# Optimization experiments

Measured on AMD Instinct MI355X. Metric: run time of the kernel, lower is better.

## Reference

```python
import math
import jax, jax.numpy as jnp
import numpy as np

L = 16
LOG2T = 19
T = 1 << LOG2T
FDIM = 2
N_MIN = 16
N_MAX = 512
N_PTS = 1 << 20
B_GROWTH = math.exp((math.log(N_MAX) - math.log(N_MIN)) / (L - 1))
RESOLUTIONS = [math.floor(N_MIN * (B_GROWTH ** i)) for i in range(L)]
BB_MIN = jnp.zeros((3,), jnp.float32)
BB_MAX = jnp.ones((3,), jnp.float32)
VERTICES = jnp.array([[0,0,0],[0,0,1],[0,1,0],[0,1,1],[1,0,0],[1,0,1],[1,1,0],[1,1,1]], dtype=jnp.uint32)
PRIMES = jnp.array([1, 2654435761, 805459861], dtype=jnp.uint32)
HASH_MASK = jnp.uint32((1 << 19) - 1)


def setup_inputs() -> dict:
    key = jax.random.key(0)
    k1, k2 = jax.random.split(key)
    xyz = jax.random.uniform(k1, (N_PTS, 3), dtype=jnp.float32)  # inside unit bb
    tables = jax.random.uniform(k2, (L, T, FDIM), dtype=jnp.float32,
                                minval=-1e-4, maxval=1e-4)
    return {"xyz": xyz, "tables": tables}


def _level(xyz, table, res):
    cell = (BB_MAX - BB_MIN) / res                                  # [3]
    min_index = jnp.floor((xyz - BB_MIN) / cell).astype(jnp.int32)  # [N,3]
    min_v = min_index.astype(jnp.float32) * cell + BB_MIN           # [N,3]
    max_v = min_v + cell
    # 8 corner indices, hash with spatial primes (wrap-around multiply == low-bit equal)
    idx = min_index[:, None, :].astype(jnp.uint32) + VERTICES       # [N,8,3]
    hp = idx * PRIMES                                               # uint32 wrap
    h = ((hp[..., 0] ^ hp[..., 1] ^ hp[..., 2]) & HASH_MASK).astype(jnp.int32)  # [N,8]
    emb = table[h]                                                  # [N,8,F] gather
    # trilinear interpolation
    d = (xyz - min_v) / (max_v - min_v)                             # [N,3]
    dx, dy, dz = d[:, 0:1], d[:, 1:2], d[:, 2:3]
    c00 = emb[:, 0] * (1 - dx) + emb[:, 4] * dx
    c01 = emb[:, 1] * (1 - dx) + emb[:, 5] * dx
    c10 = emb[:, 2] * (1 - dx) + emb[:, 6] * dx
    c11 = emb[:, 3] * (1 - dx) + emb[:, 7] * dx
    c0 = c00 * (1 - dy) + c10 * dy
    c1 = c01 * (1 - dy) + c11 * dy
    return c0 * (1 - dz) + c1 * dz                                  # [N,F]


def reference(xyz, tables):
    outs = [_level(xyz, tables[i], RESOLUTIONS[i]) for i in range(L)]
    return jnp.concatenate(outs, axis=-1)                           # [N, L*F]
```

## Files before the change

### kernel.cpp

```cpp
#include <hip/hip_runtime.h>
#include <math.h>
#include <stdint.h>

#define NLEVELS 16
#define TSIZE   (1u << 19)
#define HMASK   (TSIZE - 1u)
#define P1 2654435761u
#define P2 805459861u

typedef float v2f __attribute__((ext_vector_type(2)));
typedef float v4f __attribute__((ext_vector_type(4)));

struct LevelParams { float cell[NLEVELS]; };

__device__ __forceinline__ uint32_t bf16_rne(float f) {
    uint32_t b = __float_as_uint(f);
    return (b + 0x7FFFu + ((b >> 16) & 1u)) >> 16;
}

__global__ __launch_bounds__(256) void convert_tables_kernel(
    const v2f* __restrict__ tables, uint32_t* __restrict__ tab16,
    unsigned int nEntries)
{
    unsigned int i = blockIdx.x * 256u + threadIdx.x;
    if (i >= nEntries) return;
    v2f v = __builtin_nontemporal_load(&tables[i]);
    tab16[i] = (bf16_rne(v.x) << 16) | bf16_rne(v.y);
}

__global__ __launch_bounds__(256) void hashgrid_compute_kernel(
    const float* __restrict__ xyz,
    const uint32_t* __restrict__ tab16,
    v2f* __restrict__ stage,
    LevelParams lp,
    unsigned int npts)
{
    unsigned int b   = blockIdx.x;
    unsigned int xcd = b & 7u;
    unsigned int j   = b >> 3;
    unsigned int level = (j & 1u) ? xcd : (8u + xcd);
    unsigned int chunk = j >> 1;
    unsigned int n = chunk * 256u + threadIdx.x;

    float x = xyz[n * 3 + 0];
    float y = xyz[n * 3 + 1];
    float z = xyz[n * 3 + 2];

    float cell = lp.cell[level];

    float fx = floorf(x / cell);
    float fy = floorf(y / cell);
    float fz = floorf(z / cell);

    float mvx = fx * cell, mvy = fy * cell, mvz = fz * cell;
    float dnx = (mvx + cell) - mvx;
    float dny = (mvy + cell) - mvy;
    float dnz = (mvz + cell) - mvz;

    float dx = (x - mvx) * __builtin_amdgcn_rcpf(dnx);
    float dy = (y - mvy) * __builtin_amdgcn_rcpf(dny);
    float dz = (z - mvz) * __builtin_amdgcn_rcpf(dnz);

    unsigned int ix = (unsigned int)(int)fx;
    unsigned int iy = (unsigned int)(int)fy;
    unsigned int iz = (unsigned int)(int)fz;

    unsigned int hx0 = ix,      hx1 = ix + 1u;
    unsigned int hy0 = iy * P1, hy1 = hy0 + P1;
    unsigned int hz0 = iz * P2, hz1 = hz0 + P2;

    const uint32_t* __restrict__ tab = tab16 + (size_t)level * TSIZE;

    uint32_t u0 = tab[(hx0 ^ hy0 ^ hz0) & HMASK];
    uint32_t u1 = tab[(hx0 ^ hy0 ^ hz1) & HMASK];
    uint32_t u2 = tab[(hx0 ^ hy1 ^ hz0) & HMASK];
    uint32_t u3 = tab[(hx0 ^ hy1 ^ hz1) & HMASK];
    uint32_t u4 = tab[(hx1 ^ hy0 ^ hz0) & HMASK];
    uint32_t u5 = tab[(hx1 ^ hy0 ^ hz1) & HMASK];
    uint32_t u6 = tab[(hx1 ^ hy1 ^ hz0) & HMASK];
    uint32_t u7 = tab[(hx1 ^ hy1 ^ hz1) & HMASK];

    #define UX(u) __uint_as_float((u) & 0xFFFF0000u)
    #define UY(u) __uint_as_float((u) << 16)

    float wx0 = 1.0f - dx, wy0 = 1.0f - dy, wz0 = 1.0f - dz;

    float c00x = UX(u0) * wx0 + UX(u4) * dx;
    float c00y = UY(u0) * wx0 + UY(u4) * dx;
    float c01x = UX(u1) * wx0 + UX(u5) * dx;
    float c01y = UY(u1) * wx0 + UY(u5) * dx;
    float c10x = UX(u2) * wx0 + UX(u6) * dx;
    float c10y = UY(u2) * wx0 + UY(u6) * dx;
    float c11x = UX(u3) * wx0 + UX(u7) * dx;
    float c11y = UY(u3) * wx0 + UY(u7) * dx;

    #undef UX
    #undef UY

    float c0x = c00x * wy0 + c10x * dy;
    float c0y = c00y * wy0 + c10y * dy;
    float c1x = c01x * wy0 + c11x * dy;
    float c1y = c01y * wy0 + c11y * dy;

    v2f r;
    r.x = c0x * wz0 + c1x * dz;
    r.y = c0y * wz0 + c1y * dz;

    __builtin_nontemporal_store(r, &stage[(size_t)level * npts + n]);
}

__global__ __launch_bounds__(256) void transpose_kernel(
    const v2f* __restrict__ stage, v4f* __restrict__ out4, unsigned int npts)
{
    __shared__ v2f lds[256][17];
    unsigned int tid  = threadIdx.x;
    unsigned int base = blockIdx.x * 256u;

#pragma unroll
    for (int l = 0; l < NLEVELS; ++l)
        lds[tid][l] = __builtin_nontemporal_load(&stage[(size_t)l * npts + base + tid]);

    __syncthreads();

#pragma unroll
    for (int it = 0; it < 8; ++it) {
        unsigned int i = it * 256u + tid;
        unsigned int p = i >> 3;
        unsigned int k = i & 7u;
        v2f a = lds[p][2 * k];
        v2f c = lds[p][2 * k + 1];
        v4f w; w.x = a.x; w.y = a.y; w.z = c.x; w.w = c.y;
        __builtin_nontemporal_store(w, &out4[(size_t)blockIdx.x * 2048u + i]);
    }
}

__global__ __launch_bounds__(256) void hashgrid_direct_kernel(
    const float* __restrict__ xyz,
    const float* __restrict__ tables,
    float2* __restrict__ out,
    LevelParams lp,
    unsigned int total)
{
    unsigned int t = blockIdx.x * 256u + threadIdx.x;
    if (t >= total) return;
    unsigned int n = t >> 4;
    unsigned int l = t & 15u;

    float x = xyz[n * 3 + 0], y = xyz[n * 3 + 1], z = xyz[n * 3 + 2];
    float cell = lp.cell[l];
    float fx = floorf(x / cell), fy = floorf(y / cell), fz = floorf(z / cell);
    float mvx = fx * cell, mvy = fy * cell, mvz = fz * cell;
    float dnx = (mvx + cell) - mvx, dny = (mvy + cell) - mvy, dnz = (mvz + cell) - mvz;
    float dx = (x - mvx) * __builtin_amdgcn_rcpf(dnx);
    float dy = (y - mvy) * __builtin_amdgcn_rcpf(dny);
    float dz = (z - mvz) * __builtin_amdgcn_rcpf(dnz);
    unsigned int ix = (unsigned int)(int)fx, iy = (unsigned int)(int)fy, iz = (unsigned int)(int)fz;
    unsigned int hx0 = ix, hx1 = ix + 1u;
    unsigned int hy0 = iy * P1, hy1 = hy0 + P1;
    unsigned int hz0 = iz * P2, hz1 = hz0 + P2;
    const float2* __restrict__ tab = (const float2*)tables + (size_t)l * TSIZE;
    float2 e0 = tab[(hx0 ^ hy0 ^ hz0) & HMASK];
    float2 e1 = tab[(hx0 ^ hy0 ^ hz1) & HMASK];
    float2 e2 = tab[(hx0 ^ hy1 ^ hz0) & HMASK];
    float2 e3 = tab[(hx0 ^ hy1 ^ hz1) & HMASK];
    float2 e4 = tab[(hx1 ^ hy0 ^ hz0) & HMASK];
    float2 e5 = tab[(hx1 ^ hy0 ^ hz1) & HMASK];
    float2 e6 = tab[(hx1 ^ hy1 ^ hz0) & HMASK];
    float2 e7 = tab[(hx1 ^ hy1 ^ hz1) & HMASK];
    float wx0 = 1.0f - dx, wy0 = 1.0f - dy, wz0 = 1.0f - dz;
    float c00x = e0.x * wx0 + e4.x * dx, c00y = e0.y * wx0 + e4.y * dx;
    float c01x = e1.x * wx0 + e5.x * dx, c01y = e1.y * wx0 + e5.y * dx;
    float c10x = e2.x * wx0 + e6.x * dx, c10y = e2.y * wx0 + e6.y * dx;
    float c11x = e3.x * wx0 + e7.x * dx, c11y = e3.y * wx0 + e7.y * dx;
    float c0x = c00x * wy0 + c10x * dy, c0y = c00y * wy0 + c10y * dy;
    float c1x = c01x * wy0 + c11x * dy, c1y = c01y * wy0 + c11y * dy;
    out[t] = make_float2(c0x * wz0 + c1x * dz, c0y * wz0 + c1y * dz);
}

extern "C" void kernel_launch(void* const* d_in, const int* in_sizes, int n_in,
                              void* d_out, int out_size, void* d_ws, size_t ws_size,
                              hipStream_t stream)
{
    const float* xyz    = (const float*)d_in[0];
    const float* tables = (const float*)d_in[1];

    LevelParams lp;
    double bg = exp((log(512.0) - log(16.0)) / 15.0);
    for (int i = 0; i < NLEVELS; ++i) {
        int res = (int)floor(16.0 * pow(bg, (double)i));
        lp.cell[i] = 1.0f / (float)res;
    }

    unsigned int npts = (unsigned int)(in_sizes[0] / 3);
    size_t tabBytes   = (size_t)NLEVELS * TSIZE * 4u;
    size_t stageBytes = (size_t)npts * NLEVELS * sizeof(v2f);

    if (ws_size >= tabBytes + stageBytes && (npts & 255u) == 0u) {
        uint32_t* tab16 = (uint32_t*)d_ws;
        v2f* stage = (v2f*)((char*)d_ws + tabBytes);

        unsigned int nEntries = NLEVELS * TSIZE;
        hipLaunchKernelGGL(convert_tables_kernel,
                           dim3((nEntries + 255u) / 256u), dim3(256), 0, stream,
                           (const v2f*)tables, tab16, nEntries);

        unsigned int chunks = npts / 256u;
        hipLaunchKernelGGL(hashgrid_compute_kernel,
                           dim3(NLEVELS * chunks), dim3(256), 0, stream,
                           xyz, tab16, stage, lp, npts);

        hipLaunchKernelGGL(transpose_kernel,
                           dim3(chunks), dim3(256), 0, stream,
                           stage, (v4f*)d_out, npts);
    } else {
        unsigned int total = npts * (unsigned int)NLEVELS;
        hipLaunchKernelGGL(hashgrid_direct_kernel,
                           dim3((total + 255u) / 256u), dim3(256), 0, stream,
                           xyz, tables, (float2*)d_out, lp, total);
    }
}
```

Before: 568.5 us.

## Rebalance coarse-level work across XCDs with a per-XCD level schedule

```diff
diff --git a/kernel.cpp b/kernel.cpp
--- a/kernel.cpp
+++ b/kernel.cpp
@@ -11,7 +11,12 @@
 typedef float v2f __attribute__((ext_vector_type(2)));
 typedef float v4f __attribute__((ext_vector_type(4)));
 
-struct LevelParams { float cell[NLEVELS]; };
+struct LevelParams {
+    float    cell[NLEVELS];
+    uint32_t slvl[8][3];
+    uint32_t scnt[8][3];
+    uint32_t sbase[8][3];
+};
 
 __device__ __forceinline__ uint32_t bf16_rne(float f) {
     uint32_t b = __float_as_uint(f);
@@ -38,8 +43,18 @@
     unsigned int b   = blockIdx.x;
     unsigned int xcd = b & 7u;
     unsigned int j   = b >> 3;
-    unsigned int level = (j & 1u) ? xcd : (8u + xcd);
-    unsigned int chunk = j >> 1;
+
+    unsigned int level, chunk;
+    if (j & 1u) {
+        unsigned int t = j >> 1;
+        unsigned int s = 0;
+        while (s < 2u && t >= lp.scnt[xcd][s]) { t -= lp.scnt[xcd][s]; ++s; }
+        level = lp.slvl[xcd][s];
+        chunk = lp.sbase[xcd][s] + t;
+    } else {
+        level = 8u + xcd;
+        chunk = j >> 1;
+    }
     unsigned int n = chunk * 256u + threadIdx.x;
 
     float x = xyz[n * 3 + 0];
@@ -205,6 +220,31 @@
                            (const v2f*)tables, tab16, nEntries);
 
         unsigned int chunks = npts / 256u;
+
+        for (int x = 0; x < 8; ++x)
+            for (int s = 0; s < 3; ++s) {
+                lp.slvl[x][s] = 0; lp.scnt[x][s] = 0; lp.sbase[x][s] = 0;
+            }
+        if ((chunks & 3u) == 0u) {
+            unsigned int q = chunks / 4u;
+            for (int x = 0; x < 4; ++x) {
+                lp.slvl[x][0] = 7;         lp.scnt[x][0] = q;      lp.sbase[x][0] = (unsigned)x * q;
+                lp.slvl[x][1] = (unsigned)x; lp.scnt[x][1] = 3u * q; lp.sbase[x][1] = 0;
+            }
+            lp.slvl[4][0] = 6; lp.scnt[4][0] = 2u * q; lp.sbase[4][0] = 0;
+            lp.slvl[4][1] = 0; lp.scnt[4][1] = q;      lp.sbase[4][1] = 3u * q;
+            lp.slvl[4][2] = 1; lp.scnt[4][2] = q;      lp.sbase[4][2] = 3u * q;
+            lp.slvl[5][0] = 6; lp.scnt[5][0] = 2u * q; lp.sbase[5][0] = 2u * q;
+            lp.slvl[5][1] = 2; lp.scnt[5][1] = q;      lp.sbase[5][1] = 3u * q;
+            lp.slvl[5][2] = 3; lp.scnt[5][2] = q;      lp.sbase[5][2] = 3u * q;
+            lp.slvl[6][0] = 5; lp.scnt[6][0] = chunks; lp.sbase[6][0] = 0;
+            lp.slvl[7][0] = 4; lp.scnt[7][0] = chunks; lp.sbase[7][0] = 0;
+        } else {
+            for (int x = 0; x < 8; ++x) {
+                lp.slvl[x][0] = (unsigned)x; lp.scnt[x][0] = chunks; lp.sbase[x][0] = 0;
+            }
+        }
+
         hipLaunchKernelGGL(hashgrid_compute_kernel,
                            dim3(NLEVELS * chunks), dim3(256), 0, stream,
                            xyz, tab16, stage, lp, npts);
```

Result: faster. 544.4 us (median of 2 runs) (-4.3%).

## Fuse per-level compute and transpose into one per-point kernel over all levels

Applied to the files above, without the earlier changes.

```diff
diff --git a/kernel.cpp b/kernel.cpp
--- a/kernel.cpp
+++ b/kernel.cpp
@@ -28,109 +28,89 @@
     tab16[i] = (bf16_rne(v.x) << 16) | bf16_rne(v.y);
 }
 
-__global__ __launch_bounds__(256) void hashgrid_compute_kernel(
+__global__ __launch_bounds__(256, 4) void hashgrid_fused_kernel(
     const float* __restrict__ xyz,
     const uint32_t* __restrict__ tab16,
-    v2f* __restrict__ stage,
-    LevelParams lp,
-    unsigned int npts)
+    v4f* __restrict__ out4,
+    LevelParams lp)
 {
-    unsigned int b   = blockIdx.x;
-    unsigned int xcd = b & 7u;
-    unsigned int j   = b >> 3;
-    unsigned int level = (j & 1u) ? xcd : (8u + xcd);
-    unsigned int chunk = j >> 1;
-    unsigned int n = chunk * 256u + threadIdx.x;
+    unsigned int n = blockIdx.x * 256u + threadIdx.x;
 
     float x = xyz[n * 3 + 0];
     float y = xyz[n * 3 + 1];
     float z = xyz[n * 3 + 2];
 
-    float cell = lp.cell[level];
-
-    float fx = floorf(x / cell);
-    float fy = floorf(y / cell);
-    float fz = floorf(z / cell);
-
-    float mvx = fx * cell, mvy = fy * cell, mvz = fz * cell;
-    float dnx = (mvx + cell) - mvx;
-    float dny = (mvy + cell) - mvy;
-    float dnz = (mvz + cell) - mvz;
-
-    float dx = (x - mvx) * __builtin_amdgcn_rcpf(dnx);
-    float dy = (y - mvy) * __builtin_amdgcn_rcpf(dny);
-    float dz = (z - mvz) * __builtin_amdgcn_rcpf(dnz);
-
-    unsigned int ix = (unsigned int)(int)fx;
-    unsigned int iy = (unsigned int)(int)fy;
-    unsigned int iz = (unsigned int)(int)fz;
-
-    unsigned int hx0 = ix,      hx1 = ix + 1u;
-    unsigned int hy0 = iy * P1, hy1 = hy0 + P1;
-    unsigned int hz0 = iz * P2, hz1 = hz0 + P2;
-
-    const uint32_t* __restrict__ tab = tab16 + (size_t)level * TSIZE;
-
-    uint32_t u0 = tab[(hx0 ^ hy0 ^ hz0) & HMASK];
-    uint32_t u1 = tab[(hx0 ^ hy0 ^ hz1) & HMASK];
-    uint32_t u2 = tab[(hx0 ^ hy1 ^ hz0) & HMASK];
-    uint32_t u3 = tab[(hx0 ^ hy1 ^ hz1) & HMASK];
-    uint32_t u4 = tab[(hx1 ^ hy0 ^ hz0) & HMASK];
-    uint32_t u5 = tab[(hx1 ^ hy0 ^ hz1) & HMASK];
-    uint32_t u6 = tab[(hx1 ^ hy1 ^ hz0) & HMASK];
-    uint32_t u7 = tab[(hx1 ^ hy1 ^ hz1) & HMASK];
-
-    #define UX(u) __uint_as_float((u) & 0xFFFF0000u)
-    #define UY(u) __uint_as_float((u) << 16)
-
-    float wx0 = 1.0f - dx, wy0 = 1.0f - dy, wz0 = 1.0f - dz;
-
-    float c00x = UX(u0) * wx0 + UX(u4) * dx;
-    float c00y = UY(u0) * wx0 + UY(u4) * dx;
-    float c01x = UX(u1) * wx0 + UX(u5) * dx;
-    float c01y = UY(u1) * wx0 + UY(u5) * dx;
-    float c10x = UX(u2) * wx0 + UX(u6) * dx;
-    float c10y = UY(u2) * wx0 + UY(u6) * dx;
-    float c11x = UX(u3) * wx0 + UX(u7) * dx;
-    float c11y = UY(u3) * wx0 + UY(u7) * dx;
-
-    #undef UX
-    #undef UY
-
-    float c0x = c00x * wy0 + c10x * dy;
-    float c0y = c00y * wy0 + c10y * dy;
-    float c1x = c01x * wy0 + c11x * dy;
-    float c1y = c01y * wy0 + c11y * dy;
-
-    v2f r;
-    r.x = c0x * wz0 + c1x * dz;
-    r.y = c0y * wz0 + c1y * dz;
-
-    __builtin_nontemporal_store(r, &stage[(size_t)level * npts + n]);
-}
-
-__global__ __launch_bounds__(256) void transpose_kernel(
-    const v2f* __restrict__ stage, v4f* __restrict__ out4, unsigned int npts)
-{
-    __shared__ v2f lds[256][17];
-    unsigned int tid  = threadIdx.x;
-    unsigned int base = blockIdx.x * 256u;
+    float rx[NLEVELS], ry[NLEVELS];
 
 #pragma unroll
-    for (int l = 0; l < NLEVELS; ++l)
-        lds[tid][l] = __builtin_nontemporal_load(&stage[(size_t)l * npts + base + tid]);
+    for (int li = 0; li < NLEVELS; ++li) {
+        const int l = NLEVELS - 1 - li;
+        float cell = lp.cell[l];
 
-    __syncthreads();
+        float fx = floorf(x / cell);
+        float fy = floorf(y / cell);
+        float fz = floorf(z / cell);
+
+        float mvx = fx * cell, mvy = fy * cell, mvz = fz * cell;
+        float dnx = (mvx + cell) - mvx;
+        float dny = (mvy + cell) - mvy;
+        float dnz = (mvz + cell) - mvz;
+
+        float dx = (x - mvx) * __builtin_amdgcn_rcpf(dnx);
+        float dy = (y - mvy) * __builtin_amdgcn_rcpf(dny);
+        float dz = (z - mvz) * __builtin_amdgcn_rcpf(dnz);
+
+        unsigned int ix = (unsigned int)(int)fx;
+        unsigned int iy = (unsigned int)(int)fy;
+        unsigned int iz = (unsigned int)(int)fz;
+
+        unsigned int hx0 = ix,      hx1 = ix + 1u;
+        unsigned int hy0 = iy * P1, hy1 = hy0 + P1;
+        unsigned int hz0 = iz * P2, hz1 = hz0 + P2;
+
+        const uint32_t* __restrict__ tab = tab16 + (size_t)l * TSIZE;
+
+        uint32_t u0 = tab[(hx0 ^ hy0 ^ hz0) & HMASK];
+        uint32_t u1 = tab[(hx0 ^ hy0 ^ hz1) & HMASK];
+        uint32_t u2 = tab[(hx0 ^ hy1 ^ hz0) & HMASK];
+        uint32_t u3 = tab[(hx0 ^ hy1 ^ hz1) & HMASK];
+        uint32_t u4 = tab[(hx1 ^ hy0 ^ hz0) & HMASK];
+        uint32_t u5 = tab[(hx1 ^ hy0 ^ hz1) & HMASK];
+        uint32_t u6 = tab[(hx1 ^ hy1 ^ hz0) & HMASK];
+        uint32_t u7 = tab[(hx1 ^ hy1 ^ hz1) & HMASK];
+
+        #define UX(u) __uint_as_float((u) & 0xFFFF0000u)
+        #define UY(u) __uint_as_float((u) << 16)
+
+        float wx0 = 1.0f - dx, wy0 = 1.0f - dy, wz0 = 1.0f - dz;
+
+        float c00x = UX(u0) * wx0 + UX(u4) * dx;
+        float c00y = UY(u0) * wx0 + UY(u4) * dx;
+        float c01x = UX(u1) * wx0 + UX(u5) * dx;
+        float c01y = UY(u1) * wx0 + UY(u5) * dx;
+        float c10x = UX(u2) * wx0 + UX(u6) * dx;
+        float c10y = UY(u2) * wx0 + UY(u6) * dx;
+        float c11x = UX(u3) * wx0 + UX(u7) * dx;
+        float c11y = UY(u3) * wx0 + UY(u7) * dx;
+
+        #undef UX
+        #undef UY
+
+        float c0x = c00x * wy0 + c10x * dy;
+        float c0y = c00y * wy0 + c10y * dy;
+        float c1x = c01x * wy0 + c11x * dy;
+        float c1y = c01y * wy0 + c11y * dy;
+
+        rx[l] = c0x * wz0 + c1x * dz;
+        ry[l] = c0y * wz0 + c1y * dz;
+    }
 
 #pragma unroll
-    for (int it = 0; it < 8; ++it) {
-        unsigned int i = it * 256u + tid;
-        unsigned int p = i >> 3;
-        unsigned int k = i & 7u;
-        v2f a = lds[p][2 * k];
-        v2f c = lds[p][2 * k + 1];
-        v4f w; w.x = a.x; w.y = a.y; w.z = c.x; w.w = c.y;
-        __builtin_nontemporal_store(w, &out4[(size_t)blockIdx.x * 2048u + i]);
+    for (int k = 0; k < 8; ++k) {
+        v4f w;
+        w.x = rx[2 * k];     w.y = ry[2 * k];
+        w.z = rx[2 * k + 1]; w.w = ry[2 * k + 1];
+        __builtin_nontemporal_store(w, &out4[(size_t)n * 8u + (unsigned)k]);
     }
 }
 
@@ -192,26 +172,19 @@
     }
 
     unsigned int npts = (unsigned int)(in_sizes[0] / 3);
-    size_t tabBytes   = (size_t)NLEVELS * TSIZE * 4u;
-    size_t stageBytes = (size_t)npts * NLEVELS * sizeof(v2f);
+    size_t tabBytes = (size_t)NLEVELS * TSIZE * 4u;
 
-    if (ws_size >= tabBytes + stageBytes && (npts & 255u) == 0u) {
+    if (ws_size >= tabBytes && (npts & 255u) == 0u) {
         uint32_t* tab16 = (uint32_t*)d_ws;
-        v2f* stage = (v2f*)((char*)d_ws + tabBytes);
 
         unsigned int nEntries = NLEVELS * TSIZE;
         hipLaunchKernelGGL(convert_tables_kernel,
-                           dim3((nEntries + 255u) / 256u), dim3(256), 0, stream,
+                           dim3(nEntries / 256u), dim3(256), 0, stream,
                            (const v2f*)tables, tab16, nEntries);
 
-        unsigned int chunks = npts / 256u;
-        hipLaunchKernelGGL(hashgrid_compute_kernel,
-                           dim3(NLEVELS * chunks), dim3(256), 0, stream,
-                           xyz, tab16, stage, lp, npts);
-
-        hipLaunchKernelGGL(transpose_kernel,
-                           dim3(chunks), dim3(256), 0, stream,
-                           stage, (v4f*)d_out, npts);
+        hipLaunchKernelGGL(hashgrid_fused_kernel,
+                           dim3(npts / 256u), dim3(256), 0, stream,
+                           xyz, tab16, (v4f*)d_out, lp);
     } else {
         unsigned int total = npts * (unsigned int)NLEVELS;
         hipLaunchKernelGGL(hashgrid_direct_kernel,
```

Result: slower. 718.9 us (+26.4%).
